# Optimization experiments

Hardware: AMD Instinct MI355X
Metric: run time of the kernel (lower is better)

## Reference

```python
import jax, jax.numpy as jnp
import numpy as np

HIDDEN = 1024
NUM_HEADS = 16
HOP_NUM = 1023  # seq_len = hop_num + 1 = 1024
ATT_SIZE = HIDDEN // NUM_HEADS
SCALE = ATT_SIZE ** (-0.5)
B, S = 8, HOP_NUM + 1


def setup_inputs() -> dict:
    key = jax.random.key(0)
    ks = jax.random.split(key, 13)
    lim = 1.0 / np.sqrt(HIDDEN)
    return {
        "q": jax.random.normal(ks[0], (B, S, HIDDEN), jnp.float32),
        "k": jax.random.normal(ks[1], (B, S, HIDDEN), jnp.float32),
        "v": jax.random.normal(ks[2], (B, S, HIDDEN), jnp.float32),
        "attn_bias": jax.random.normal(ks[3], (B, 1, S, S), jnp.float32),
        "Wq": jax.random.uniform(ks[4], (HIDDEN, HIDDEN), jnp.float32, -lim, lim),
        "bq": jax.random.uniform(ks[5], (HIDDEN,), jnp.float32, -lim, lim),
        "Wk": jax.random.uniform(ks[6], (HIDDEN, HIDDEN), jnp.float32, -lim, lim),
        "bk": jax.random.uniform(ks[7], (HIDDEN,), jnp.float32, -lim, lim),
        "Wv": jax.random.uniform(ks[8], (HIDDEN, HIDDEN), jnp.float32, -lim, lim),
        "bv": jax.random.uniform(ks[9], (HIDDEN,), jnp.float32, -lim, lim),
        "Wo": jax.random.uniform(ks[10], (HIDDEN, HIDDEN), jnp.float32, -lim, lim),
        "bo": jax.random.uniform(ks[11], (HIDDEN,), jnp.float32, -lim, lim),
        "zoom_bias": jax.random.normal(ks[12], (2 * HOP_NUM + 1, 1), jnp.float32),
    }


def reference(q, k, v, attn_bias, Wq, bq, Wk, bk, Wv, bv, Wo, bo, zoom_bias):
    b, s, _ = q.shape
    # projections -> [b, s, h, d]
    qh = (q @ Wq.T + bq).reshape(b, s, NUM_HEADS, ATT_SIZE)
    kh = (k @ Wk.T + bk).reshape(b, s, NUM_HEADS, ATT_SIZE)
    vh = (v @ Wv.T + bv).reshape(b, s, NUM_HEADS, ATT_SIZE)
    # relative zoom encoding: ze[i, j] = zoom_bias[i - j + hop_num]
    idx = jnp.arange(s)[:, None] - jnp.arange(s)[None, :] + HOP_NUM
    ze = zoom_bias[idx, 0]  # [s, s]
    # scaled dot-product attention with additive zoom bias
    scores = jnp.einsum("bshd,bthd->bhst", qh * SCALE, kh) + ze + attn_bias
    probs = jax.nn.softmax(scores, axis=-1)
    out = jnp.einsum("bhst,bthd->bshd", probs, vh).reshape(b, s, NUM_HEADS * ATT_SIZE)
    return out @ Wo.T + bo
```

## Files before the change

### kernel.cpp

```cpp
#include <hip/hip_runtime.h>
#include <cstdint>


#define SQ   1024
#define HID  1024
#define CEXP 0.18033688f
#define LOG2E 1.44269504f

typedef __attribute__((ext_vector_type(8))) __bf16 bf16x8;
typedef __attribute__((ext_vector_type(8))) unsigned short ushort8;
typedef __attribute__((ext_vector_type(4))) float  floatx4;

__device__ __forceinline__ float b2f(unsigned short x) {
    return __builtin_bit_cast(float, (uint32_t)x << 16);
}
__device__ __forceinline__ unsigned short f2bf(float f) {
    uint32_t u = __builtin_bit_cast(uint32_t, f);
    u += 0x7fffu + ((u >> 16) & 1u);
    return (unsigned short)(u >> 16);
}

__device__ __forceinline__ void glds16(const void* g, void* l) {
    __builtin_amdgcn_global_load_lds(
        (const __attribute__((address_space(1))) void*)g,
        (__attribute__((address_space(3))) void*)l, 16, 0, 0);
}

__global__ void cvt(const float* __restrict__ s, unsigned short* __restrict__ d,
                    int n4, float scale) {
    const int i = blockIdx.x * blockDim.x + threadIdx.x;
    if (i >= n4) return;
    const floatx4 v = *(const floatx4*)(s + 4 * (size_t)i);
    uint32_t lo = (uint32_t)f2bf(v[0] * scale) | ((uint32_t)f2bf(v[1] * scale) << 16);
    uint32_t hi = (uint32_t)f2bf(v[2] * scale) | ((uint32_t)f2bf(v[3] * scale) << 16);
    ((uint2*)d)[i] = make_uint2(lo, hi);
}

__global__ void cvt3(const float* __restrict__ s0, const float* __restrict__ s1,
                     const float* __restrict__ s2, unsigned short* __restrict__ d0,
                     unsigned short* __restrict__ d1, unsigned short* __restrict__ d2,
                     int n4) {
    const int i = blockIdx.x * blockDim.x + threadIdx.x;
    if (i >= n4) return;
    const int z = blockIdx.y;
    const float* s = z == 0 ? s0 : (z == 1 ? s1 : s2);
    unsigned short* d = z == 0 ? d0 : (z == 1 ? d1 : d2);
    const floatx4 v = *(const floatx4*)(s + 4 * (size_t)i);
    uint32_t lo = (uint32_t)f2bf(v[0]) | ((uint32_t)f2bf(v[1]) << 16);
    uint32_t hi = (uint32_t)f2bf(v[2]) | ((uint32_t)f2bf(v[3]) << 16);
    ((uint2*)d)[i] = make_uint2(lo, hi);
}

__global__ __launch_bounds__(256) void gemm_qkv(
    const short* __restrict__ Aq, const short* __restrict__ Ak,
    const short* __restrict__ Av, const short* __restrict__ Wq_,
    const short* __restrict__ Wk_, const short* __restrict__ Wv_,
    const float* __restrict__ bq_, const float* __restrict__ bk_,
    const float* __restrict__ bv_, short* __restrict__ oq,
    short* __restrict__ ok, short* __restrict__ ov)
{
    __shared__ __align__(16) short As[4096];
    __shared__ __align__(16) short Bs[4096];

    const int z = blockIdx.z;
    const short* A    = z == 0 ? Aq  : (z == 1 ? Ak  : Av);
    const short* Bw   = z == 0 ? Wq_ : (z == 1 ? Wk_ : Wv_);
    const float* bias = z == 0 ? bq_ : (z == 1 ? bk_ : bv_);
    short* C          = z == 0 ? oq  : (z == 1 ? ok  : ov);
    const bool trans  = (z == 2);

    const int tid = threadIdx.x;
    const int w = tid >> 6, lane = tid & 63;
    const int quad = lane >> 4, c = lane & 15;
    const int wr = w >> 1, wc = w & 1;

    const int nwg = gridDim.x * gridDim.y;
    const int id  = blockIdx.y * gridDim.x + blockIdx.x;
    const int nid = (id & 7) * (nwg >> 3) + (id >> 3);
    const int bn = nid & 7, bm = nid >> 3;

    const short* ag0 = A  + (size_t)(bm * 128 + w * 16 + c) * HID + quad * 8;
    const short* ag1 = ag0 + (size_t)64 * HID;
    const short* bg0 = Bw + (size_t)(bn * 128 + w * 16 + c) * HID + quad * 8;
    const short* bg1 = bg0 + (size_t)64 * HID;

    floatx4 acc[4][4] = {};

    for (int kt = 0; kt < 32; ++kt) {
        __syncthreads();
        glds16(ag0, As + w * 512);
        glds16(ag1, As + (w + 4) * 512);
        glds16(bg0, Bs + w * 512);
        glds16(bg1, Bs + (w + 4) * 512);
        asm volatile("s_waitcnt vmcnt(0)" ::: "memory");
        __syncthreads();
        ag0 += 32; ag1 += 32; bg0 += 32; bg1 += 32;

        bf16x8 a[4], b[4];
#pragma unroll
        for (int i = 0; i < 4; ++i)
            a[i] = *(const bf16x8*)(As + (wr * 4 + i) * 512 + lane * 8);
#pragma unroll
        for (int j = 0; j < 4; ++j)
            b[j] = *(const bf16x8*)(Bs + (wc * 4 + j) * 512 + lane * 8);
#pragma unroll
        for (int i = 0; i < 4; ++i)
#pragma unroll
            for (int j = 0; j < 4; ++j)
                acc[i][j] = __builtin_amdgcn_mfma_f32_16x16x32_bf16(a[i], b[j], acc[i][j], 0, 0, 0);
    }

    float bsv[4];
#pragma unroll
    for (int j = 0; j < 4; ++j)
        bsv[j] = bias[bn * 128 + wc * 64 + j * 16 + c];

#pragma unroll
    for (int i = 0; i < 4; ++i) {
#pragma unroll
        for (int j = 0; j < 4; ++j) {
            const int n = bn * 128 + wc * 64 + j * 16 + c;
#pragma unroll
            for (int r = 0; r < 4; ++r) {
                const int row = bm * 128 + wr * 64 + i * 16 + quad * 4 + r;
                const float val = acc[i][j][r] + bsv[j];
                const size_t idx = trans
                    ? ((size_t)(row >> 10) * HID + n) * SQ + (row & 1023)
                    : (size_t)row * HID + n;
                C[idx] = (short)f2bf(val);
            }
        }
    }
}

__global__ __launch_bounds__(256) void gemm_bt(
    const short* __restrict__ A, const short* __restrict__ Bw,
    const float* __restrict__ bias, float* __restrict__ C, size_t cOff)
{
    __shared__ __align__(16) short As[4096];
    __shared__ __align__(16) short Bs[4096];

    const int tid = threadIdx.x;
    const int w = tid >> 6, lane = tid & 63;
    const int quad = lane >> 4, c = lane & 15;
    const int wr = w >> 1, wc = w & 1;

    const int nwg = gridDim.x * gridDim.y;
    const int id  = blockIdx.y * gridDim.x + blockIdx.x;
    const int nid = (id & 7) * (nwg >> 3) + (id >> 3);
    const int bn = nid & 7, bm = nid >> 3;

    const short* ag0 = A  + (size_t)(bm * 128 + w * 16 + c) * HID + quad * 8;
    const short* ag1 = ag0 + (size_t)64 * HID;
    const short* bg0 = Bw + (size_t)(bn * 128 + w * 16 + c) * HID + quad * 8;
    const short* bg1 = bg0 + (size_t)64 * HID;

    floatx4 acc[4][4] = {};

    for (int kt = 0; kt < 32; ++kt) {
        __syncthreads();
        glds16(ag0, As + w * 512);
        glds16(ag1, As + (w + 4) * 512);
        glds16(bg0, Bs + w * 512);
        glds16(bg1, Bs + (w + 4) * 512);
        asm volatile("s_waitcnt vmcnt(0)" ::: "memory");
        __syncthreads();
        ag0 += 32; ag1 += 32; bg0 += 32; bg1 += 32;

        bf16x8 a[4], b[4];
#pragma unroll
        for (int i = 0; i < 4; ++i)
            a[i] = *(const bf16x8*)(As + (wr * 4 + i) * 512 + lane * 8);
#pragma unroll
        for (int j = 0; j < 4; ++j)
            b[j] = *(const bf16x8*)(Bs + (wc * 4 + j) * 512 + lane * 8);
#pragma unroll
        for (int i = 0; i < 4; ++i)
#pragma unroll
            for (int j = 0; j < 4; ++j)
                acc[i][j] = __builtin_amdgcn_mfma_f32_16x16x32_bf16(a[i], b[j], acc[i][j], 0, 0, 0);
    }

    float bsv[4];
#pragma unroll
    for (int j = 0; j < 4; ++j)
        bsv[j] = bias[bn * 128 + wc * 64 + j * 16 + c];

#pragma unroll
    for (int i = 0; i < 4; ++i)
#pragma unroll
        for (int j = 0; j < 4; ++j) {
            const int n = bn * 128 + wc * 64 + j * 16 + c;
#pragma unroll
            for (int r = 0; r < 4; ++r) {
                const int row = bm * 128 + wr * 64 + i * 16 + quad * 4 + r;
                C[cOff + (size_t)row * HID + n] = acc[i][j][r] + bsv[j];
            }
        }
}

__global__ __launch_bounds__(256) void attn(
    const short* __restrict__ qh, const short* __restrict__ kh,
    const short* __restrict__ vht, const unsigned short* __restrict__ abc,
    const float* __restrict__ zbf, short* __restrict__ aout, int b0)
{
    __shared__ __align__(16) short Kf[4096];
    __shared__ __align__(16) short Vf[4096];
    __shared__ __align__(16) short Ps[4][2304];
    __shared__ float Zs[1152];

    const int tid = threadIdx.x;
    const int w = tid >> 6, lane = tid & 63;
    const int quad = lane >> 4, c = lane & 15;
    const int qb = blockIdx.x, h = blockIdx.y, bl = blockIdx.z;
    const int b = b0 + bl;

    for (int j = tid; j < 1151; j += 256)
        Zs[j] = zbf[qb * 128 + j] * LOG2E;

    const size_t blS = (size_t)bl * SQ;

    bf16x8 qa[2][2];
#pragma unroll
    for (int m = 0; m < 2; ++m)
#pragma unroll
        for (int half = 0; half < 2; ++half)
            qa[m][half] = *(const bf16x8*)(qh + (blS + qb * 128 + w * 32 + m * 16 + c) * HID
                                               + h * 64 + half * 32 + quad * 8);

    const short* kg = kh  + (blS + 2 * c + (w & 1)) * HID + h * 64 + (w >> 1) * 32 + quad * 8;
    const short* vg = vht + ((size_t)bl * HID + h * 64 + w * 16 + c) * SQ + quad * 8;
    const size_t bge = ((size_t)b * SQ + qb * 128 + w * 32 + quad * 4) * SQ;

    bf16x8 kv0 = *(const bf16x8*)kg, kv1 = *(const bf16x8*)(kg + 32 * HID);
    bf16x8 vv0 = *(const bf16x8*)vg, vv1 = *(const bf16x8*)(vg + 32);

    uint32_t bp[2][4][2];
    auto loadB = [&](int K0) {
#pragma unroll
        for (int m = 0; m < 2; ++m)
#pragma unroll
            for (int r = 0; r < 4; ++r)
#pragma unroll
                for (int sub = 0; sub < 2; ++sub)
                    bp[m][r][sub] = *(const uint32_t*)(abc + bge + (size_t)(m * 16 + r) * SQ
                                                        + K0 + sub * 32 + 2 * c);
    };
    loadB(0);

    floatx4 o[2][4] = {};
    float sume[2][4] = {};

    for (int kt = 0; kt < 16; ++kt) {
        __syncthreads();
        *(bf16x8*)(Kf + w * 512 + lane * 8)       = kv0;
        *(bf16x8*)(Kf + (w + 4) * 512 + lane * 8) = kv1;
        *(bf16x8*)(Vf + w * 512 + lane * 8)       = vv0;
        *(bf16x8*)(Vf + (w + 4) * 512 + lane * 8) = vv1;
        __syncthreads();

        if (kt < 15) {
            kg += 64 * HID; vg += 64;
            kv0 = *(const bf16x8*)kg; kv1 = *(const bf16x8*)(kg + 32 * HID);
            vv0 = *(const bf16x8*)vg; vv1 = *(const bf16x8*)(vg + 32);
        }

        floatx4 sc[2][2][2] = {};
#pragma unroll
        for (int sub = 0; sub < 2; ++sub) {
            bf16x8 kf[2][2];
#pragma unroll
            for (int half = 0; half < 2; ++half)
#pragma unroll
                for (int kb = 0; kb < 2; ++kb)
                    kf[half][kb] = *(const bf16x8*)(Kf + (sub * 4 + half * 2 + kb) * 512 + lane * 8);
#pragma unroll
            for (int m = 0; m < 2; ++m)
#pragma unroll
                for (int kb = 0; kb < 2; ++kb) {
                    sc[m][sub][kb] = __builtin_amdgcn_mfma_f32_16x16x32_bf16(qa[m][0], kf[0][kb], sc[m][sub][kb], 0, 0, 0);
                    sc[m][sub][kb] = __builtin_amdgcn_mfma_f32_16x16x32_bf16(qa[m][1], kf[1][kb], sc[m][sub][kb], 0, 0, 0);
                }
        }

        const int k0 = kt * 64;
#pragma unroll
        for (int m = 0; m < 2; ++m) {
#pragma unroll
            for (int r = 0; r < 4; ++r) {
                const int lrq = w * 32 + m * 16 + quad * 4 + r;
                const int tb = lrq + 1023 - k0;
#pragma unroll
                for (int sub = 0; sub < 2; ++sub) {
                    const int kl = sub * 32 + 2 * c;
                    const uint32_t bv_ = bp[m][r][sub];
                    const float z0 = Zs[tb - kl], z1 = Zs[tb - kl - 1];
                    const float s0 = sc[m][sub][0][r] * CEXP + z0 + b2f((unsigned short)(bv_ & 0xffffu));
                    const float s1 = sc[m][sub][1][r] * CEXP + z1
                                   + __builtin_bit_cast(float, bv_ & 0xffff0000u);
                    const float e0 = __builtin_amdgcn_exp2f(s0);
                    const float e1 = __builtin_amdgcn_exp2f(s1);
                    sume[m][r] += e0 + e1;
                    const uint32_t pp = (uint32_t)f2bf(e0) | ((uint32_t)f2bf(e1) << 16);
                    *(uint32_t*)(&Ps[w][0] + (m * 16 + quad * 4 + r) * 72 + kl) = pp;
                }
            }
        }

        if (kt < 15) loadB(k0 + 64);

#pragma unroll
        for (int sub = 0; sub < 2; ++sub) {
            bf16x8 ap[2];
#pragma unroll
            for (int m = 0; m < 2; ++m)
                ap[m] = *(const bf16x8*)(&Ps[w][0] + (m * 16 + c) * 72 + sub * 32 + quad * 8);
#pragma unroll
            for (int dt = 0; dt < 4; ++dt) {
                const bf16x8 vf = *(const bf16x8*)(Vf + (sub * 4 + dt) * 512 + lane * 8);
#pragma unroll
                for (int m = 0; m < 2; ++m)
                    o[m][dt] = __builtin_amdgcn_mfma_f32_16x16x32_bf16(ap[m], vf, o[m][dt], 0, 0, 0);
            }
        }
    }

#pragma unroll
    for (int m = 0; m < 2; ++m)
#pragma unroll
        for (int r = 0; r < 4; ++r) {
            float s = sume[m][r];
            s += __shfl_xor(s, 1);
            s += __shfl_xor(s, 2);
            s += __shfl_xor(s, 4);
            s += __shfl_xor(s, 8);
            sume[m][r] = 1.0f / s;
        }

#pragma unroll
    for (int m = 0; m < 2; ++m)
#pragma unroll
        for (int dt = 0; dt < 4; ++dt)
#pragma unroll
            for (int r = 0; r < 4; ++r) {
                const size_t row = blS + qb * 128 + w * 32 + m * 16 + quad * 4 + r;
                ((unsigned short*)aout)[row * HID + h * 64 + dt * 16 + c] =
                    f2bf(o[m][dt][r] * sume[m][r]);
            }
}

extern "C" void kernel_launch(void* const* d_in, const int* in_sizes, int n_in,
                              void* d_out, int out_size, void* d_ws, size_t ws_size,
                              hipStream_t stream) {
    const float* q  = (const float*)d_in[0];
    const float* k  = (const float*)d_in[1];
    const float* v  = (const float*)d_in[2];
    const float* ab = (const float*)d_in[3];
    const float* Wq = (const float*)d_in[4];  const float* bq = (const float*)d_in[5];
    const float* Wk = (const float*)d_in[6];  const float* bk = (const float*)d_in[7];
    const float* Wv = (const float*)d_in[8];  const float* bv = (const float*)d_in[9];
    const float* Wo = (const float*)d_in[10]; const float* bo = (const float*)d_in[11];
    const float* zb = (const float*)d_in[12];

    const size_t perB = (size_t)SQ * HID;
    const size_t WN   = (size_t)HID * HID;

    int G = 8;
    while (G > 1 && 24ull * 1024 * 1024 + 12ull * G * perB > ws_size) G >>= 1;

    unsigned short* Wqc = (unsigned short*)d_ws;
    unsigned short* Wkc = Wqc + WN;
    unsigned short* Wvc = Wkc + WN;
    unsigned short* Woc = Wvc + WN;
    unsigned short* abc = Woc + WN;
    short* cbq = (short*)(abc + 8 * perB);
    short* cbk = cbq + (size_t)G * perB;
    short* cbv = cbk + (size_t)G * perB;
    short* qh  = cbv + (size_t)G * perB;
    short* khp = qh  + (size_t)G * perB;
    short* vht = khp + (size_t)G * perB;
    short* ao  = cbq;

    const dim3 bt(256);
    const int ngroups = 8 / G;
    const int cn4 = (int)(G * perB / 4);
    const int cgrid = (cn4 + 255) / 256;

    cvt<<<(WN / 4 + 255) / 256, 256, 0, stream>>>(Wq, Wqc, WN / 4, 1.0f);
    cvt<<<(WN / 4 + 255) / 256, 256, 0, stream>>>(Wk, Wkc, WN / 4, 1.0f);
    cvt<<<(WN / 4 + 255) / 256, 256, 0, stream>>>(Wv, Wvc, WN / 4, 1.0f);
    cvt<<<(WN / 4 + 255) / 256, 256, 0, stream>>>(Wo, Woc, WN / 4, 1.0f);
    cvt<<<(8 * perB / 4 + 255) / 256, 256, 0, stream>>>(ab, abc, 8 * perB / 4, LOG2E);

    for (int g = 0; g < ngroups; ++g) {
        const size_t off = (size_t)g * G * perB;
        cvt3<<<dim3(cgrid, 3), 256, 0, stream>>>(
            q + off, k + off, v + off,
            (unsigned short*)cbq, (unsigned short*)cbk, (unsigned short*)cbv, cn4);
        gemm_qkv<<<dim3(8, G * 8, 3), bt, 0, stream>>>(
            cbq, cbk, cbv, (short*)Wqc, (short*)Wkc, (short*)Wvc,
            bq, bk, bv, qh, khp, vht);
        attn<<<dim3(8, 16, G), bt, 0, stream>>>(qh, khp, vht, abc, zb, ao, g * G);
        gemm_bt<<<dim3(8, G * 8), bt, 0, stream>>>(ao, (short*)Woc, bo, (float*)d_out, off);
    }
}
```

Baseline: 421.0 us.

## Remap attention blocks across batch/head, raise MFMA wave priority, merge weight conversions

The attention kernel now remaps its block index when the grid covers all 8 batches, so that consecutively scheduled blocks span several heads and batches, which changes L2 and cache locality across CUs. It also wraps the two MFMA phases in s_setprio(1)/s_setprio(0) so waves issuing matrix instructions are favored over waves in the softmax/exp phase. The four weight-conversion launches are merged into one 2D-grid kernel to cut launch overhead. These are independent tweaks; the remap only applies when G equals 8.

```diff
diff --git a/kernel.cpp b/kernel.cpp
--- a/kernel.cpp
+++ b/kernel.cpp
@@ -51,6 +51,22 @@
     ((uint2*)d)[i] = make_uint2(lo, hi);
 }
 
+__global__ void cvt4(const float* __restrict__ s0, const float* __restrict__ s1,
+                     const float* __restrict__ s2, const float* __restrict__ s3,
+                     unsigned short* __restrict__ d0, unsigned short* __restrict__ d1,
+                     unsigned short* __restrict__ d2, unsigned short* __restrict__ d3,
+                     int n4) {
+    const int i = blockIdx.x * blockDim.x + threadIdx.x;
+    if (i >= n4) return;
+    const int z = blockIdx.y;
+    const float* s = z == 0 ? s0 : (z == 1 ? s1 : (z == 2 ? s2 : s3));
+    unsigned short* d = z == 0 ? d0 : (z == 1 ? d1 : (z == 2 ? d2 : d3));
+    const floatx4 v = *(const floatx4*)(s + 4 * (size_t)i);
+    uint32_t lo = (uint32_t)f2bf(v[0]) | ((uint32_t)f2bf(v[1]) << 16);
+    uint32_t hi = (uint32_t)f2bf(v[2]) | ((uint32_t)f2bf(v[3]) << 16);
+    ((uint2*)d)[i] = make_uint2(lo, hi);
+}
+
 __global__ __launch_bounds__(256) void gemm_qkv(
     const short* __restrict__ Aq, const short* __restrict__ Ak,
     const short* __restrict__ Av, const short* __restrict__ Wq_,
@@ -212,7 +228,15 @@
     const int tid = threadIdx.x;
     const int w = tid >> 6, lane = tid & 63;
     const int quad = lane >> 4, c = lane & 15;
-    const int qb = blockIdx.x, h = blockIdx.y, bl = blockIdx.z;
+
+    int qb, h, bl;
+    if (gridDim.z == 8) {
+        const int B = blockIdx.x + (blockIdx.y << 3) + (blockIdx.z << 7);
+        const int hb = (B >> 6) * 8 + (B & 7);
+        qb = (B >> 3) & 7; h = hb & 15; bl = hb >> 4;
+    } else {
+        qb = blockIdx.x; h = blockIdx.y; bl = blockIdx.z;
+    }
     const int b = b0 + bl;
 
     for (int j = tid; j < 1151; j += 256)
@@ -266,6 +290,7 @@
         }
 
         floatx4 sc[2][2][2] = {};
+        __builtin_amdgcn_s_setprio(1);
 #pragma unroll
         for (int sub = 0; sub < 2; ++sub) {
             bf16x8 kf[2][2];
@@ -282,6 +307,7 @@
                     sc[m][sub][kb] = __builtin_amdgcn_mfma_f32_16x16x32_bf16(qa[m][1], kf[1][kb], sc[m][sub][kb], 0, 0, 0);
                 }
         }
+        __builtin_amdgcn_s_setprio(0);
 
         const int k0 = kt * 64;
 #pragma unroll
@@ -309,6 +335,7 @@
 
         if (kt < 15) loadB(k0 + 64);
 
+        __builtin_amdgcn_s_setprio(1);
 #pragma unroll
         for (int sub = 0; sub < 2; ++sub) {
             bf16x8 ap[2];
@@ -323,6 +350,7 @@
                     o[m][dt] = __builtin_amdgcn_mfma_f32_16x16x32_bf16(ap[m], vf, o[m][dt], 0, 0, 0);
             }
         }
+        __builtin_amdgcn_s_setprio(0);
     }
 
 #pragma unroll
@@ -386,10 +414,8 @@
     const int cn4 = (int)(G * perB / 4);
     const int cgrid = (cn4 + 255) / 256;
 
-    cvt<<<(WN / 4 + 255) / 256, 256, 0, stream>>>(Wq, Wqc, WN / 4, 1.0f);
-    cvt<<<(WN / 4 + 255) / 256, 256, 0, stream>>>(Wk, Wkc, WN / 4, 1.0f);
-    cvt<<<(WN / 4 + 255) / 256, 256, 0, stream>>>(Wv, Wvc, WN / 4, 1.0f);
-    cvt<<<(WN / 4 + 255) / 256, 256, 0, stream>>>(Wo, Woc, WN / 4, 1.0f);
+    cvt4<<<dim3((WN / 4 + 255) / 256, 4), 256, 0, stream>>>(
+        Wq, Wk, Wv, Wo, Wqc, Wkc, Wvc, Woc, (int)(WN / 4));
     cvt<<<(8 * perB / 4 + 255) / 256, 256, 0, stream>>>(ab, abc, 8 * perB / 4, LOG2E);
 
     for (int g = 0; g < ngroups; ++g) {
```

Measured after the change: 415.0 us. No clear change (-1.4%).
